# Performance work log

Measured on AMD Instinct MI355X. Metric: run time of the kernel, lower is better.

Reference implementation:

```python
import jax, jax.numpy as jnp
import numpy as np

N, D, P = 131072, 128, 512
COMMIT_W = 0.1
ENT_LAMBDA = 200000.0


def setup_inputs() -> dict:
    key = jax.random.key(0)
    k1, k2 = jax.random.split(key)
    input_data = jax.random.normal(k1, (N, D), dtype=jnp.float32)
    # codebook init matches torch: uniform(-1/p, 1/p)
    codebook = jax.random.uniform(k2, (P, D), dtype=jnp.float32, minval=-1.0 / P, maxval=1.0 / P)
    return {"input_data": input_data, "codebook": codebook}


def _inv_cov(codebook):
    # full covariance of codebook rows (torch.no_grad -> stop_gradient)
    p, d = codebook.shape
    mu = codebook.mean(axis=0, keepdims=True)
    c = codebook - mu
    cov = (c.T @ c) / (p - 1) + 1e-3 * jnp.eye(d, dtype=codebook.dtype)
    return jax.lax.stop_gradient(jnp.linalg.inv(cov))


def reference(input_data, codebook):
    p, d = codebook.shape
    inv_cov = _inv_cov(codebook)

    # Mahalanobis distances via quadratic-form expansion (no [N,p,d] intermediate):
    xS = input_data @ inv_cov                      # [N, d]
    xq = jnp.sum(xS * input_data, axis=1)          # [N]
    cS = codebook @ inv_cov                        # [p, d]
    cq = jnp.sum(cS * codebook, axis=1)            # [p]
    distances = xq[:, None] - 2.0 * (xS @ codebook.T) + cq[None, :]  # [N, p]

    idx = jnp.argmin(distances, axis=1)            # [N]
    quantized = jnp.take(codebook, idx, axis=0)    # [N, d] (== one_hot @ codebook)

    def batch_mahal(x, y):
        diff = x - y
        return jnp.mean(jnp.sum((diff @ inv_cov) * diff, axis=1))

    codebook_loss = batch_mahal(jax.lax.stop_gradient(quantized), input_data)
    commitment_loss = COMMIT_W * batch_mahal(quantized, jax.lax.stop_gradient(input_data))

    # codebook usage entropy regularizer
    counts = jnp.zeros((p,), dtype=input_data.dtype).at[idx].add(1.0)
    probs = counts / (counts.sum() + 1e-8)
    entropy = -jnp.sum(probs * jnp.log(probs + 1e-8))
    codebook_loss = codebook_loss - ENT_LAMBDA * entropy

    # straight-through estimator
    quantized_st = input_data + jax.lax.stop_gradient(quantized - input_data)
    return quantized_st, commitment_loss, codebook_loss, idx
```

## Files before the change

### kernel.cpp

```cpp
#include <hip/hip_runtime.h>


typedef _Float16 half8 __attribute__((ext_vector_type(8)));
typedef float floatx4 __attribute__((ext_vector_type(4)));

#define NROWS 131072
#define DIM 128
#define NCODE 512
#define ND 16777216

#define WS_LH    0
#define WS_CH    32768
#define WS_W     163840
#define WS_SH    294912
#define WS_CQ    327680
#define WS_CNT   329728
#define WS_SUMS  346112

#define MFMA16(A, B, C) __builtin_amdgcn_mfma_f32_16x16x32_f16(A, B, C, 0, 0, 0)

__device__ __forceinline__ int moff(int row, int colh) {
  return row * 256 + ((((row & 7) << 4) ^ (colh * 2)));
}

__global__ __launch_bounds__(256) void k_prep1(
    const float* __restrict__ cb, _Float16* __restrict__ Lh,
    unsigned* __restrict__ cnt, float* __restrict__ sums) {
  __shared__ float mu[128];
  __shared__ float red[256];
  __shared__ float colI[2][512];
  __shared__ float csh[2];

  const int t = threadIdx.x, b = blockIdx.x;
  const int j = t & 127, h = t >> 7;

  if (b < 8) {
    cnt[b * 512 + t] = 0u;
    cnt[b * 512 + 256 + t] = 0u;
  }
  if (b == 8) sums[t] = 0.f;

  float sm = 0.f, sf = 0.f;
  for (int p = 0; p < 256; ++p) {
    float v = cb[(h * 256 + p) * DIM + j];
    sm += v;
    sf += v * v;
  }
  red[t] = sm;
  for (int k = t; k < 1024; k += 256)
    colI[k >> 9][k & 511] = cb[(k & 511) * DIM + 2 * b + (k >> 9)];
  __syncthreads();
  if (t < 128) mu[t] = (red[t] + red[t + 128]) * (1.f / 512.f);
  __syncthreads();
  red[t] = sf - ((t < 128) ? 512.f * mu[t] * mu[t] : 0.f);
  __syncthreads();
  for (int k = 128; k > 0; k >>= 1) {
    if (t < k) red[t] += red[t + k];
    __syncthreads();
  }
  if (t == 0) {
    float tr = red[0] * (1.f / 511.f) + 0.128f;
    csh[0] = 128.f / tr;
    csh[1] = sqrtf(128.f / tr);
  }
  __syncthreads();
  const float c = csh[0], rc = csh[1];

  const int i = 2 * b + h;
  float g = 0.f;
  for (int q = 0; q < 512; ++q) g += colI[h][q] * cb[q * DIM + j];
  float lv = rc * (((i == j) ? (1.5f - 5e-4f * c) : 0.f) -
                   (c / 1022.f) * (g - 512.f * mu[i] * mu[j]));
  *(_Float16*)((char*)Lh + moff(i, j)) = (_Float16)lv;
}

__global__ __launch_bounds__(256) void k_prep23(
    const float* __restrict__ cb, const _Float16* __restrict__ Lh,
    _Float16* __restrict__ Ch, _Float16* __restrict__ W,
    _Float16* __restrict__ Sh, float* __restrict__ cqb) {
  __shared__ float cqpart[16][4];
  const int t = threadIdx.x;
  const int w = t >> 6, lane = t & 63, quad = lane >> 4, l16 = lane & 15;

  if (blockIdx.x >= 32) {
    const int p0 = (blockIdx.x - 32) * 16;
    half8 a[4];
#pragma unroll
    for (int ci = 0; ci < 4; ++ci)
      a[ci] = *(const half8*)((const char*)Lh + moff(p0 + l16, ci * 32 + quad * 8));
#pragma unroll
    for (int t2 = 0; t2 < 2; ++t2) {
      const int tile = w * 2 + t2;
      floatx4 s = {0.f, 0.f, 0.f, 0.f};
#pragma unroll
      for (int ci = 0; ci < 4; ++ci) {
        half8 bb = *(const half8*)((const char*)Lh +
                                   moff(tile * 16 + l16, ci * 32 + quad * 8));
        s = MFMA16(a[ci], bb, s);
      }
#pragma unroll
      for (int r = 0; r < 4; ++r)
        *(_Float16*)((char*)Sh + moff(p0 + quad * 4 + r, tile * 16 + l16)) =
            (_Float16)s[r];
    }
    return;
  }

  const int p0 = blockIdx.x * 16;

  half8 a[4];
#pragma unroll
  for (int ci = 0; ci < 4; ++ci) {
    const float4* v = (const float4*)(cb + (p0 + l16) * DIM + ci * 32 + quad * 8);
    float4 v0 = v[0], v1 = v[1];
    half8 hh;
    hh[0] = (_Float16)v0.x; hh[1] = (_Float16)v0.y;
    hh[2] = (_Float16)v0.z; hh[3] = (_Float16)v0.w;
    hh[4] = (_Float16)v1.x; hh[5] = (_Float16)v1.y;
    hh[6] = (_Float16)v1.z; hh[7] = (_Float16)v1.w;
    a[ci] = hh;
  }
  float sq[4] = {0.f, 0.f, 0.f, 0.f};
#pragma unroll
  for (int t2 = 0; t2 < 2; ++t2) {
    const int tile = w * 2 + t2;
    floatx4 s = {0.f, 0.f, 0.f, 0.f};
#pragma unroll
    for (int ci = 0; ci < 4; ++ci) {
      half8 bb = *(const half8*)((const char*)Lh +
                                 moff(tile * 16 + l16, ci * 32 + quad * 8));
      s = MFMA16(a[ci], bb, s);
    }
#pragma unroll
    for (int r = 0; r < 4; ++r) {
      *(_Float16*)((char*)Ch + moff(p0 + quad * 4 + r, tile * 16 + l16)) =
          (_Float16)s[r];
      sq[r] += s[r] * s[r];
    }
  }
#pragma unroll
  for (int r = 0; r < 4; ++r) {
    float v = sq[r];
    v += __shfl_xor(v, 1); v += __shfl_xor(v, 2);
    v += __shfl_xor(v, 4); v += __shfl_xor(v, 8);
    sq[r] = v;
  }
  if (l16 == 0)
#pragma unroll
    for (int r = 0; r < 4; ++r) cqpart[quad * 4 + r][w] = sq[r];
  __syncthreads();
  if (t < 16)
    cqb[p0 + t] = 1024.f - 0.5f * (cqpart[t][0] + cqpart[t][1] +
                                   cqpart[t][2] + cqpart[t][3]);

  half8 a2[4];
#pragma unroll
  for (int ci = 0; ci < 4; ++ci)
    a2[ci] = *(const half8*)((const char*)Ch + moff(p0 + l16, ci * 32 + quad * 8));
#pragma unroll
  for (int t2 = 0; t2 < 2; ++t2) {
    const int tile = w * 2 + t2;
    floatx4 s = {0.f, 0.f, 0.f, 0.f};
#pragma unroll
    for (int ci = 0; ci < 4; ++ci) {
      half8 bb = *(const half8*)((const char*)Lh +
                                 moff(tile * 16 + l16, ci * 32 + quad * 8));
      s = MFMA16(a2[ci], bb, s);
    }
#pragma unroll
    for (int r = 0; r < 4; ++r)
      *(_Float16*)((char*)W + moff(p0 + quad * 4 + r, tile * 16 + l16)) =
          (_Float16)s[r];
  }
}

__global__ __launch_bounds__(1024, 4) void k_main(
    const float* __restrict__ X, const float* __restrict__ cb,
    const _Float16* __restrict__ Sh, const _Float16* __restrict__ W,
    const float* __restrict__ cqb, float* __restrict__ out,
    unsigned* __restrict__ cnt, float* __restrict__ sums) {
  __shared__ __align__(16) char Ws[131072];

  const int tid = threadIdx.x;
  const int w = tid >> 6, lane = tid & 63;
  const int quad = lane >> 4, l16 = lane & 15;
  const int R0 = blockIdx.x * 512 + w * 32;
  const int rep = blockIdx.x & 7;

  half8 a0[4], a1[4];
#pragma unroll
  for (int ci = 0; ci < 4; ++ci) {
    const float4* p0 = (const float4*)(X + (size_t)(R0 + l16) * DIM + ci * 32 + quad * 8);
    float4 u0 = p0[0], u1 = p0[1];
    half8 h;
    h[0] = (_Float16)u0.x; h[1] = (_Float16)u0.y;
    h[2] = (_Float16)u0.z; h[3] = (_Float16)u0.w;
    h[4] = (_Float16)u1.x; h[5] = (_Float16)u1.y;
    h[6] = (_Float16)u1.z; h[7] = (_Float16)u1.w;
    a0[ci] = h;
    const float4* p1 = (const float4*)(X + (size_t)(R0 + 16 + l16) * DIM + ci * 32 + quad * 8);
    float4 w0 = p1[0], w1 = p1[1];
    h[0] = (_Float16)w0.x; h[1] = (_Float16)w0.y;
    h[2] = (_Float16)w0.z; h[3] = (_Float16)w0.w;
    h[4] = (_Float16)w1.x; h[5] = (_Float16)w1.y;
    h[6] = (_Float16)w1.z; h[7] = (_Float16)w1.w;
    a1[ci] = h;
  }

  const char* WB = (const char*)W;
#pragma unroll
  for (int i = 0; i < 8; ++i)
    __builtin_amdgcn_global_load_lds(
        (const __attribute__((address_space(1))) void*)(WB + i * 16384 + w * 1024 + lane * 16),
        (__attribute__((address_space(3))) void*)(Ws + i * 16384 + w * 1024),
        16, 0, 0);

  float y2 = 0.f;
  const char* ShB = (const char*)Sh;
  for (int v = 0; v < 8; ++v) {
    half8 bb[4];
#pragma unroll
    for (int ci = 0; ci < 4; ++ci)
      bb[ci] = *(const half8*)(ShB + moff(v * 16 + l16, ci * 32 + quad * 8));
    floatx4 s0a = {0.f, 0.f, 0.f, 0.f}, s0b = {0.f, 0.f, 0.f, 0.f};
    floatx4 s1a = {0.f, 0.f, 0.f, 0.f}, s1b = {0.f, 0.f, 0.f, 0.f};
    s0a = MFMA16(a0[0], bb[0], s0a); s0b = MFMA16(a0[1], bb[1], s0b);
    s1a = MFMA16(a1[0], bb[0], s1a); s1b = MFMA16(a1[1], bb[1], s1b);
    s0a = MFMA16(a0[2], bb[2], s0a); s0b = MFMA16(a0[3], bb[3], s0b);
    s1a = MFMA16(a1[2], bb[2], s1a); s1b = MFMA16(a1[3], bb[3], s1b);
    const int col = v * 16 + l16;
#pragma unroll
    for (int r = 0; r < 4; ++r) {
      float xv0 = X[(size_t)(R0 + quad * 4 + r) * DIM + col];
      float xv1 = X[(size_t)(R0 + 16 + quad * 4 + r) * DIM + col];
      y2 += (s0a[r] + s0b[r]) * xv0 + (s1a[r] + s1b[r]) * xv1;
    }
  }

  __syncthreads();

  float m0[4] = {0.f, 0.f, 0.f, 0.f}, m1[4] = {0.f, 0.f, 0.f, 0.f};
  float iv = cqb[l16];
  for (int t = 0; t < 32; ++t) {
    half8 bb[4];
#pragma unroll
    for (int ci = 0; ci < 4; ++ci)
      bb[ci] = *(const half8*)(Ws + moff(t * 16 + l16, ci * 32 + quad * 8));
    float ivn = (t < 31) ? cqb[(t + 1) * 16 + l16] : 0.f;
    floatx4 s0a = {iv, iv, iv, iv}, s0b = {0.f, 0.f, 0.f, 0.f};
    floatx4 s1a = {iv, iv, iv, iv}, s1b = {0.f, 0.f, 0.f, 0.f};
    __builtin_amdgcn_s_setprio(1);
    s0a = MFMA16(a0[0], bb[0], s0a); s0b = MFMA16(a0[1], bb[1], s0b);
    s1a = MFMA16(a1[0], bb[0], s1a); s1b = MFMA16(a1[1], bb[1], s1b);
    s0a = MFMA16(a0[2], bb[2], s0a); s0b = MFMA16(a0[3], bb[3], s0b);
    s1a = MFMA16(a1[2], bb[2], s1a); s1b = MFMA16(a1[3], bb[3], s1b);
    __builtin_amdgcn_s_setprio(0);
    const unsigned tag = 511u - (unsigned)(t * 16 + l16);
#pragma unroll
    for (int r = 0; r < 4; ++r) {
      float v0 = s0a[r] + s0b[r], v1 = s1a[r] + s1b[r];
      unsigned u0 = ((__float_as_uint(v0) + 0x100u) & 0xFFFFFE00u) | tag;
      unsigned u1 = ((__float_as_uint(v1) + 0x100u) & 0xFFFFFE00u) | tag;
      m0[r] = fmaxf(m0[r], __uint_as_float(u0));
      m1[r] = fmaxf(m1[r], __uint_as_float(u1));
    }
    iv = ivn;
  }

#pragma unroll
  for (int r = 0; r < 4; ++r) {
#pragma unroll
    for (int msk = 1; msk < 16; msk <<= 1) {
      m0[r] = fmaxf(m0[r], __shfl_xor(m0[r], msk));
      m1[r] = fmaxf(m1[r], __shfl_xor(m1[r], msk));
    }
  }

  float contrib = y2;
  if (l16 == 0) {
#pragma unroll
    for (int r = 0; r < 4; ++r) {
      contrib -= 2.f * (__uint_as_float(__float_as_uint(m0[r]) & 0xFFFFFE00u) - 1024.f);
      contrib -= 2.f * (__uint_as_float(__float_as_uint(m1[r]) & 0xFFFFFE00u) - 1024.f);
    }
  }
#pragma unroll
  for (int msk = 1; msk < 64; msk <<= 1) contrib += __shfl_xor(contrib, msk);
  if (lane == 0) unsafeAtomicAdd(&sums[rep * 32], contrib);

  {
    const float4* cb4 = (const float4*)cb;
    float4* out4 = (float4*)out;
#pragma unroll
    for (int r = 0; r < 4; ++r) {
      const int j0 = 511 - (int)(__float_as_uint(m0[r]) & 511u);
      const int j1 = 511 - (int)(__float_as_uint(m1[r]) & 511u);
      const int row0 = R0 + quad * 4 + r, row1 = row0 + 16;
      out4[(size_t)row0 * 32 + l16 * 2]     = cb4[(size_t)j0 * 32 + l16 * 2];
      out4[(size_t)row0 * 32 + l16 * 2 + 1] = cb4[(size_t)j0 * 32 + l16 * 2 + 1];
      out4[(size_t)row1 * 32 + l16 * 2]     = cb4[(size_t)j1 * 32 + l16 * 2];
      out4[(size_t)row1 * 32 + l16 * 2 + 1] = cb4[(size_t)j1 * 32 + l16 * 2 + 1];
      if (l16 == 0) {
        out[ND + 2 + row0] = (float)j0;
        out[ND + 2 + row1] = (float)j1;
        atomicAdd(&cnt[rep * 512 + j0], 1u);
        atomicAdd(&cnt[rep * 512 + j1], 1u);
      }
    }
  }
}

__global__ void k_final(const unsigned* __restrict__ cnt,
                        const float* __restrict__ sums, float* __restrict__ out) {
  __shared__ double sd[256];
  int t = threadIdx.x;
  double e = 0.0;
  for (int c = t; c < NCODE; c += 256) {
    unsigned u = 0;
#pragma unroll
    for (int r = 0; r < 8; ++r) u += cnt[r * 512 + c];
    float p = (float)u * (1.0f / 131072.0f);
    e += (double)(p * logf(p + 1e-8f));
  }
  sd[t] = e;
  __syncthreads();
  for (int k = 128; k > 0; k >>= 1) {
    if (t < k) sd[t] += sd[t + k];
    __syncthreads();
  }
  if (t == 0) {
    double ent = -sd[0];
    float st = 0.f;
#pragma unroll
    for (int r = 0; r < 8; ++r) st += sums[r * 32];
    double M = (double)st / 131072.0;
    out[ND] = (float)(0.1 * M);
    out[ND + 1] = (float)(M - 200000.0 * ent);
  }
}

extern "C" void kernel_launch(void* const* d_in, const int* in_sizes, int n_in,
                              void* d_out, int out_size, void* d_ws, size_t ws_size,
                              hipStream_t stream) {
  const float* X = (const float*)d_in[0];
  const float* cb = (const float*)d_in[1];
  char* ws = (char*)d_ws;
  _Float16* Lh = (_Float16*)(ws + WS_LH);
  _Float16* Ch = (_Float16*)(ws + WS_CH);
  _Float16* W = (_Float16*)(ws + WS_W);
  _Float16* Sh = (_Float16*)(ws + WS_SH);
  float* cqb = (float*)(ws + WS_CQ);
  unsigned* cnt = (unsigned*)(ws + WS_CNT);
  float* sums = (float*)(ws + WS_SUMS);
  float* out = (float*)d_out;

  k_prep1<<<64, 256, 0, stream>>>(cb, Lh, cnt, sums);
  k_prep23<<<40, 256, 0, stream>>>(cb, Lh, Ch, W, Sh, cqb);
  k_main<<<256, 1024, 0, stream>>>(X, cb, Sh, W, cqb, out, cnt, sums);
  k_final<<<1, 256, 0, stream>>>(cnt, sums, out);
}
```

Before: 167.0 us.

## Stage X tile in LDS as fp16 and fuse final reduction via last-block ticket

Each wave now loads its 32 rows of X once, converts them to fp16 and stores them in a swizzled LDS region. The MFMA A-operands and the per-element x values for the quadratic form are then read from LDS instead of re-reading global X. The W codebook-transform load into LDS is deferred until after this phase because it reuses the same LDS space. The separate k_final launch is removed: a global atomic ticket lets the last block compute the entropy and final losses, which saves one kernel launch at the cost of a threadfence and an atomic per block.

```diff
diff --git a/kernel.cpp b/kernel.cpp
--- a/kernel.cpp
+++ b/kernel.cpp
@@ -2,6 +2,7 @@
 
 
 typedef _Float16 half8 __attribute__((ext_vector_type(8)));
+typedef _Float16 half4 __attribute__((ext_vector_type(4)));
 typedef float floatx4 __attribute__((ext_vector_type(4)));
 
 #define NROWS 131072
@@ -16,6 +17,7 @@
 #define WS_CQ    327680
 #define WS_CNT   329728
 #define WS_SUMS  346112
+#define WS_TICK  347136
 
 #define MFMA16(A, B, C) __builtin_amdgcn_mfma_f32_16x16x32_f16(A, B, C, 0, 0, 0)
 
@@ -25,7 +27,8 @@
 
 __global__ __launch_bounds__(256) void k_prep1(
     const float* __restrict__ cb, _Float16* __restrict__ Lh,
-    unsigned* __restrict__ cnt, float* __restrict__ sums) {
+    unsigned* __restrict__ cnt, float* __restrict__ sums,
+    unsigned* __restrict__ tick) {
   __shared__ float mu[128];
   __shared__ float red[256];
   __shared__ float colI[2][512];
@@ -39,6 +42,7 @@
     cnt[b * 512 + 256 + t] = 0u;
   }
   if (b == 8) sums[t] = 0.f;
+  if (b == 9 && t == 0) tick[0] = 0u;
 
   float sm = 0.f, sf = 0.f;
   for (int p = 0; p < 256; ++p) {
@@ -178,42 +182,38 @@
     const float* __restrict__ X, const float* __restrict__ cb,
     const _Float16* __restrict__ Sh, const _Float16* __restrict__ W,
     const float* __restrict__ cqb, float* __restrict__ out,
-    unsigned* __restrict__ cnt, float* __restrict__ sums) {
+    unsigned* __restrict__ cnt, float* __restrict__ sums,
+    unsigned* __restrict__ tick) {
   __shared__ __align__(16) char Ws[131072];
+  __shared__ unsigned lastflag;
 
   const int tid = threadIdx.x;
   const int w = tid >> 6, lane = tid & 63;
   const int quad = lane >> 4, l16 = lane & 15;
   const int R0 = blockIdx.x * 512 + w * 32;
   const int rep = blockIdx.x & 7;
+  char* Xw = Ws + w * 8192;
+
+  {
+    const float4* src = (const float4*)(X + (size_t)R0 * DIM);
+#pragma unroll
+    for (int i = 0; i < 16; ++i) {
+      int g = i * 64 + lane;
+      int row = g >> 5, c4 = g & 31;
+      float4 v = src[g];
+      half4 h;
+      h[0] = (_Float16)v.x; h[1] = (_Float16)v.y;
+      h[2] = (_Float16)v.z; h[3] = (_Float16)v.w;
+      *(half4*)(Xw + moff(row, c4 * 4)) = h;
+    }
+  }
 
   half8 a0[4], a1[4];
 #pragma unroll
   for (int ci = 0; ci < 4; ++ci) {
-    const float4* p0 = (const float4*)(X + (size_t)(R0 + l16) * DIM + ci * 32 + quad * 8);
-    float4 u0 = p0[0], u1 = p0[1];
-    half8 h;
-    h[0] = (_Float16)u0.x; h[1] = (_Float16)u0.y;
-    h[2] = (_Float16)u0.z; h[3] = (_Float16)u0.w;
-    h[4] = (_Float16)u1.x; h[5] = (_Float16)u1.y;
-    h[6] = (_Float16)u1.z; h[7] = (_Float16)u1.w;
-    a0[ci] = h;
-    const float4* p1 = (const float4*)(X + (size_t)(R0 + 16 + l16) * DIM + ci * 32 + quad * 8);
-    float4 w0 = p1[0], w1 = p1[1];
-    h[0] = (_Float16)w0.x; h[1] = (_Float16)w0.y;
-    h[2] = (_Float16)w0.z; h[3] = (_Float16)w0.w;
-    h[4] = (_Float16)w1.x; h[5] = (_Float16)w1.y;
-    h[6] = (_Float16)w1.z; h[7] = (_Float16)w1.w;
-    a1[ci] = h;
-  }
-
-  const char* WB = (const char*)W;
-#pragma unroll
-  for (int i = 0; i < 8; ++i)
-    __builtin_amdgcn_global_load_lds(
-        (const __attribute__((address_space(1))) void*)(WB + i * 16384 + w * 1024 + lane * 16),
-        (__attribute__((address_space(3))) void*)(Ws + i * 16384 + w * 1024),
-        16, 0, 0);
+    a0[ci] = *(const half8*)(Xw + moff(l16, ci * 32 + quad * 8));
+    a1[ci] = *(const half8*)(Xw + moff(16 + l16, ci * 32 + quad * 8));
+  }
 
   float y2 = 0.f;
   const char* ShB = (const char*)Sh;
@@ -231,12 +231,23 @@
     const int col = v * 16 + l16;
 #pragma unroll
     for (int r = 0; r < 4; ++r) {
-      float xv0 = X[(size_t)(R0 + quad * 4 + r) * DIM + col];
-      float xv1 = X[(size_t)(R0 + 16 + quad * 4 + r) * DIM + col];
+      float xv0 = (float)*(const _Float16*)(Xw + moff(quad * 4 + r, col));
+      float xv1 = (float)*(const _Float16*)(Xw + moff(16 + quad * 4 + r, col));
       y2 += (s0a[r] + s0b[r]) * xv0 + (s1a[r] + s1b[r]) * xv1;
     }
   }
 
+  asm volatile("s_waitcnt lgkmcnt(0)" ::: "memory");
+  __builtin_amdgcn_sched_barrier(0);
+  {
+    const char* WB = (const char*)W;
+#pragma unroll
+    for (int i = 0; i < 8; ++i)
+      __builtin_amdgcn_global_load_lds(
+          (const __attribute__((address_space(1))) void*)(WB + w * 8192 + i * 1024 + lane * 16),
+          (__attribute__((address_space(3))) void*)(Ws + w * 8192 + i * 1024),
+          16, 0, 0);
+  }
   __syncthreads();
 
   float m0[4] = {0.f, 0.f, 0.f, 0.f}, m1[4] = {0.f, 0.f, 0.f, 0.f};
@@ -308,34 +319,39 @@
       }
     }
   }
-}
-
-__global__ void k_final(const unsigned* __restrict__ cnt,
-                        const float* __restrict__ sums, float* __restrict__ out) {
-  __shared__ double sd[256];
-  int t = threadIdx.x;
-  double e = 0.0;
-  for (int c = t; c < NCODE; c += 256) {
-    unsigned u = 0;
-#pragma unroll
-    for (int r = 0; r < 8; ++r) u += cnt[r * 512 + c];
-    float p = (float)u * (1.0f / 131072.0f);
-    e += (double)(p * logf(p + 1e-8f));
-  }
-  sd[t] = e;
-  __syncthreads();
-  for (int k = 128; k > 0; k >>= 1) {
-    if (t < k) sd[t] += sd[t + k];
+
+  __threadfence();
+  __syncthreads();
+  if (tid == 0) {
+    unsigned old = atomicAdd(tick, 1u);
+    lastflag = (old == 255u) ? 1u : 0u;
+  }
+  __syncthreads();
+  if (lastflag) {
+    double* sd = (double*)Ws;
+    double e = 0.0;
+    if (tid < 512) {
+      unsigned u = 0;
+#pragma unroll
+      for (int r = 0; r < 8; ++r) u += cnt[r * 512 + tid];
+      float p = (float)u * (1.0f / 131072.0f);
+      e = (double)(p * logf(p + 1e-8f));
+      sd[tid] = e;
+    }
     __syncthreads();
-  }
-  if (t == 0) {
-    double ent = -sd[0];
-    float st = 0.f;
-#pragma unroll
-    for (int r = 0; r < 8; ++r) st += sums[r * 32];
-    double M = (double)st / 131072.0;
-    out[ND] = (float)(0.1 * M);
-    out[ND + 1] = (float)(M - 200000.0 * ent);
+    for (int k = 256; k > 0; k >>= 1) {
+      if (tid < k) sd[tid] += sd[tid + k];
+      __syncthreads();
+    }
+    if (tid == 0) {
+      double ent = -sd[0];
+      float st = 0.f;
+#pragma unroll
+      for (int r = 0; r < 8; ++r) st += sums[r * 32];
+      double M = (double)st / 131072.0;
+      out[ND] = (float)(0.1 * M);
+      out[ND + 1] = (float)(M - 200000.0 * ent);
+    }
   }
 }
 
@@ -352,10 +368,10 @@
   float* cqb = (float*)(ws + WS_CQ);
   unsigned* cnt = (unsigned*)(ws + WS_CNT);
   float* sums = (float*)(ws + WS_SUMS);
+  unsigned* tick = (unsigned*)(ws + WS_TICK);
   float* out = (float*)d_out;
 
-  k_prep1<<<64, 256, 0, stream>>>(cb, Lh, cnt, sums);
+  k_prep1<<<64, 256, 0, stream>>>(cb, Lh, cnt, sums, tick);
   k_prep23<<<40, 256, 0, stream>>>(cb, Lh, Ch, W, Sh, cqb);
-  k_main<<<256, 1024, 0, stream>>>(X, cb, Sh, W, cqb, out, cnt, sums);
-  k_final<<<1, 256, 0, stream>>>(cnt, sums, out);
-}
+  k_main<<<256, 1024, 0, stream>>>(X, cb, Sh, W, cqb, out, cnt, sums, tick);
+}
```

New measurement: 444.4 us. 2.66x slower.
